# Kernel tuning notes

Hardware: AMD Instinct MI355X
Metric: run time of the kernel (lower is better)

Reference implementation:

```python
import jax, jax.numpy as jnp
import numpy as np

U, H, R, N = 128, 5120, 160, 32  # users, d_inner, dt_rank, d_state(padded)


def setup_inputs() -> dict:
    key = jax.random.key(0)
    ks = jax.random.split(key, 8)
    s_in = 1.0 / np.sqrt(H)
    s_r = 1.0 / np.sqrt(R)
    x = jax.random.normal(ks[0], (1, 1, U, H), dtype=jnp.float32)
    h_prev = jnp.zeros((U, H, N), dtype=jnp.float32)
    W_dt_low = jax.random.normal(ks[1], (H, R), dtype=jnp.float32) * s_in
    W_dt = jax.random.normal(ks[2], (R, H), dtype=jnp.float32) * s_r
    b_dt = jax.random.normal(ks[3], (H,), dtype=jnp.float32) * 0.1
    W_B = jax.random.normal(ks[4], (H, N), dtype=jnp.float32) * s_in
    W_C = jax.random.normal(ks[5], (H, N), dtype=jnp.float32) * s_in
    # A = -exp(A_log): strictly negative, as in Mamba preprocessing
    A = -jnp.exp(jax.random.normal(ks[6], (H, N), dtype=jnp.float32) * 0.5)
    D = jax.random.normal(ks[7], (H,), dtype=jnp.float32)
    return {"x": x, "h_prev": h_prev, "W_dt_low": W_dt_low, "W_dt": W_dt,
            "b_dt": b_dt, "W_B": W_B, "W_C": W_C, "A": A, "D": D}


def reference(x, h_prev, W_dt_low, W_dt, b_dt, W_B, W_C, A, D):
    xf = x[0, 0]                                        # (U, H)
    # delta: low-rank projection then dt_proj + bias, softplus (beta=1, thresh=20)
    z = (xf @ W_dt_low) @ W_dt + b_dt                    # (U, H)
    delta = jnp.where(z > 20.0, z, jax.nn.softplus(z))   # (U, H)
    B = xf @ W_B                                         # (U, N)
    C = xf @ W_C                                         # (U, N)
    # discretized recurrence: h' = exp(delta*A)*h + delta*B*x
    abar = jnp.exp(delta[:, :, None] * A[None])          # (U, H, N)
    h_new = abar * h_prev + delta[:, :, None] * B[:, None, :] * xf[:, :, None]
    y = jnp.einsum('uhn,un->uh', h_new, C)               # (U, H)
    out = xf * D[None, :] + y                            # (U, H)
    return out[None, None]                               # (1, 1, U, H)
```

## Files before the change

### kernel.cpp

```cpp
#include <hip/hip_runtime.h>

#define UU 128
#define HH 5120
#define RR 160
#define NS 32

__global__ __launch_bounds__(256) void ka_proj(const float* __restrict__ x,
                                               const float* __restrict__ Wdl,
                                               const float* __restrict__ WB,
                                               const float* __restrict__ WC,
                                               float* __restrict__ dtlP,
                                               float* __restrict__ bcP) {
    const int ut = blockIdx.x >> 5;
    const int hc = blockIdx.x & 31;
    const int u0 = ut * 8;
    const int h0 = hc * 160;
    const int t  = threadIdx.x;
    __shared__ __attribute__((aligned(16))) float xs[160 * 8];
    #pragma unroll
    for (int k = 0; k < 5; ++k) {
        int i  = t + k * 256;
        int ul = i / 160, hh = i % 160;
        xs[hh * 8 + ul] = x[(u0 + ul) * HH + h0 + hh];
    }
    __syncthreads();
    const int c = t;
    const float* wp;
    int stride;
    float* outp = nullptr;
    if (c < 160) {
        wp = Wdl + (size_t)h0 * RR + c;          stride = RR;
        outp = dtlP + hc * (RR * UU) + c * UU + u0;
    } else if (c < 224) {
        int col = c - 160;
        wp = ((col < 32) ? WB : WC) + (size_t)h0 * NS + (col & 31);
        stride = NS;
        outp = bcP + hc * (64 * UU) + col * UU + u0;
    } else {
        wp = Wdl; stride = 0;
    }
    float a[8] = {0.f, 0.f, 0.f, 0.f, 0.f, 0.f, 0.f, 0.f};
    #pragma unroll 4
    for (int hh = 0; hh < 160; ++hh) {
        float w = wp[hh * stride];
        float4 x0 = *(const float4*)&xs[hh * 8];
        float4 x1 = *(const float4*)&xs[hh * 8 + 4];
        a[0] += x0.x * w; a[1] += x0.y * w; a[2] += x0.z * w; a[3] += x0.w * w;
        a[4] += x1.x * w; a[5] += x1.y * w; a[6] += x1.z * w; a[7] += x1.w * w;
    }
    if (outp) {
        *(float4*)&outp[0] = make_float4(a[0], a[1], a[2], a[3]);
        *(float4*)&outp[4] = make_float4(a[4], a[5], a[6], a[7]);
    }
}

__global__ __launch_bounds__(256) void kb_delta(const float* __restrict__ dtlP,
                                                const float* __restrict__ Wdt,
                                                const float* __restrict__ bdt,
                                                const float* __restrict__ bcP,
                                                float* __restrict__ BC,
                                                float* __restrict__ delta) {
    const int ut = blockIdx.x / 20;
    const int ht = blockIdx.x % 20;
    const int u0 = ut * 8, h0 = ht * 256, t = threadIdx.x;
    __shared__ __attribute__((aligned(16))) float dtl[RR * 8];
    #pragma unroll
    for (int k = 0; k < 5; ++k) {
        int i = t + k * 256;
        int r = i >> 3, ul = i & 7;
        float s = 0.f;
        #pragma unroll
        for (int hc = 0; hc < 32; ++hc)
            s += dtlP[hc * (RR * UU) + r * UU + u0 + ul];
        dtl[i] = s;
    }
    if (ht == 0) {
        #pragma unroll
        for (int k = 0; k < 2; ++k) {
            int i = t + k * 256;
            int ul = i >> 6, col = i & 63;
            float s = 0.f;
            #pragma unroll
            for (int hc = 0; hc < 32; ++hc)
                s += bcP[hc * (64 * UU) + col * UU + u0 + ul];
            BC[(u0 + ul) * 64 + col] = s;
        }
    }
    __syncthreads();
    const int h = h0 + t;
    float acc[8] = {0.f, 0.f, 0.f, 0.f, 0.f, 0.f, 0.f, 0.f};
    #pragma unroll 4
    for (int r = 0; r < RR; ++r) {
        float w = Wdt[(size_t)r * HH + h];
        float4 a = *(const float4*)&dtl[r * 8];
        float4 b = *(const float4*)&dtl[r * 8 + 4];
        acc[0] += a.x * w; acc[1] += a.y * w; acc[2] += a.z * w; acc[3] += a.w * w;
        acc[4] += b.x * w; acc[5] += b.y * w; acc[6] += b.z * w; acc[7] += b.w * w;
    }
    const float bv = bdt[h];
    #pragma unroll
    for (int ul = 0; ul < 8; ++ul) {
        float z = acc[ul] + bv;
        float d = (z > 20.f) ? z : __logf(1.f + __expf(z));
        delta[(size_t)(u0 + ul) * HH + h] = d;
    }
}

__global__ __launch_bounds__(256) void kc_main(const float* __restrict__ x,
                                               const float* __restrict__ hprev,
                                               const float* __restrict__ A,
                                               const float* __restrict__ Dp,
                                               const float* __restrict__ BC,
                                               const float* __restrict__ delta,
                                               float* __restrict__ out) {
    const int u  = blockIdx.x / 20;
    const int ht = blockIdx.x % 20;
    const int t  = threadIdx.x;
    __shared__ __attribute__((aligned(16))) float bc[64];
    if (t < 64) bc[t] = BC[u * 64 + t];
    __syncthreads();
    const int h = ht * 256 + t;
    const float d  = delta[(size_t)u * HH + h];
    const float xv = x[(size_t)u * HH + h];
    const float dx = d * xv;
    const float4* hp = (const float4*)&hprev[((size_t)u * HH + h) * NS];
    const float4* ap = (const float4*)&A[(size_t)h * NS];
    float y = 0.f;
    #pragma unroll
    for (int j = 0; j < 8; ++j) {
        float4 a4 = ap[j];
        float4 h4 = hp[j];
        float4 b4 = *(const float4*)&bc[j * 4];
        float4 c4 = *(const float4*)&bc[32 + j * 4];
        float n0 = __expf(d * a4.x) * h4.x + dx * b4.x;
        float n1 = __expf(d * a4.y) * h4.y + dx * b4.y;
        float n2 = __expf(d * a4.z) * h4.z + dx * b4.z;
        float n3 = __expf(d * a4.w) * h4.w + dx * b4.w;
        y += n0 * c4.x + n1 * c4.y + n2 * c4.z + n3 * c4.w;
    }
    out[(size_t)u * HH + h] = xv * Dp[h] + y;
}

extern "C" void kernel_launch(void* const* d_in, const int* in_sizes, int n_in,
                              void* d_out, int out_size, void* d_ws, size_t ws_size,
                              hipStream_t stream) {
    const float* x     = (const float*)d_in[0];
    const float* hprev = (const float*)d_in[1];
    const float* Wdl   = (const float*)d_in[2];
    const float* Wdt   = (const float*)d_in[3];
    const float* bdt   = (const float*)d_in[4];
    const float* WB    = (const float*)d_in[5];
    const float* WC    = (const float*)d_in[6];
    const float* A     = (const float*)d_in[7];
    const float* Dp    = (const float*)d_in[8];
    float* out = (float*)d_out;
    float* ws  = (float*)d_ws;

    float* dtlP  = ws;
    float* bcP   = ws + 655360;
    float* BC    = ws + 917504;
    float* delta = ws + 925696;

    ka_proj <<<512,  256, 0, stream>>>(x, Wdl, WB, WC, dtlP, bcP);
    kb_delta<<<320,  256, 0, stream>>>(dtlP, Wdt, bdt, bcP, BC, delta);
    kc_main <<<2560, 256, 0, stream>>>(x, hprev, A, Dp, BC, delta, out);
}
```

Measured before the change: 214.9 us.

## Split each state row across 8 lanes in the scan kernel for coalesced loads

In the main recurrence kernel, each h row of 32 states is now handled by 8 lanes, each loading one float4 of h_prev and A, and the partial dot products with C are combined by xor shuffles. Before, each thread read a whole 128-byte row, so a wave's loads were strided across rows. Now adjacent lanes read contiguous memory, which should coalesce the dominant h_prev stream. The cost is redundant loads of delta, x and D by 8 lanes, the shuffle reduction, and only one lane in eight writing each output.

```diff
diff --git a/kernel.cpp b/kernel.cpp
--- a/kernel.cpp
+++ b/kernel.cpp
@@ -119,26 +119,29 @@
     __shared__ __attribute__((aligned(16))) float bc[64];
     if (t < 64) bc[t] = BC[u * 64 + t];
     __syncthreads();
-    const int h = ht * 256 + t;
-    const float d  = delta[(size_t)u * HH + h];
-    const float xv = x[(size_t)u * HH + h];
-    const float dx = d * xv;
-    const float4* hp = (const float4*)&hprev[((size_t)u * HH + h) * NS];
-    const float4* ap = (const float4*)&A[(size_t)h * NS];
-    float y = 0.f;
+    const int g = t >> 3;
+    const int l = t & 7;
+    const float4 b4 = *(const float4*)&bc[l * 4];
+    const float4 c4 = *(const float4*)&bc[32 + l * 4];
     #pragma unroll
-    for (int j = 0; j < 8; ++j) {
-        float4 a4 = ap[j];
-        float4 h4 = hp[j];
-        float4 b4 = *(const float4*)&bc[j * 4];
-        float4 c4 = *(const float4*)&bc[32 + j * 4];
-        float n0 = __expf(d * a4.x) * h4.x + dx * b4.x;
-        float n1 = __expf(d * a4.y) * h4.y + dx * b4.y;
-        float n2 = __expf(d * a4.z) * h4.z + dx * b4.z;
-        float n3 = __expf(d * a4.w) * h4.w + dx * b4.w;
-        y += n0 * c4.x + n1 * c4.y + n2 * c4.z + n3 * c4.w;
+    for (int i = 0; i < 8; ++i) {
+        const int h = ht * 256 + i * 32 + g;
+        const float d  = delta[(size_t)u * HH + h];
+        const float xv = x[(size_t)u * HH + h];
+        const float4 a4 = *(const float4*)&A[(size_t)h * NS + l * 4];
+        const float4 hp = *(const float4*)&hprev[((size_t)u * HH + h) * NS + l * 4];
+        const float dx = d * xv;
+        float4 hn;
+        hn.x = __expf(d * a4.x) * hp.x + dx * b4.x;
+        hn.y = __expf(d * a4.y) * hp.y + dx * b4.y;
+        hn.z = __expf(d * a4.z) * hp.z + dx * b4.z;
+        hn.w = __expf(d * a4.w) * hp.w + dx * b4.w;
+        float y = hn.x * c4.x + hn.y * c4.y + hn.z * c4.z + hn.w * c4.w;
+        y += __shfl_xor(y, 1);
+        y += __shfl_xor(y, 2);
+        y += __shfl_xor(y, 4);
+        if (l == 0) out[(size_t)u * HH + h] = xv * Dp[h] + y;
     }
-    out[(size_t)u * HH + h] = xv * Dp[h] + y;
 }
 
 extern "C" void kernel_launch(void* const* d_in, const int* in_sizes, int n_in,
```

Result: faster. 207.1 us (-3.6%).
